# Kernel optimization log

Measured on AMD Instinct MI355X. Metric: run time of the kernel, lower is better.

## Reference

```python
import jax, jax.numpy as jnp
import numpy as np

B, N, K, H, HEADS = 4, 2000, 30, 128, 4
D = H // HEADS  # per-head dim = 32
NUM_IN = 2 * H
NEG_INF = jnp.float32(np.finfo(np.float32).min)


def setup_inputs() -> dict:
    key = jax.random.key(0)
    ks = jax.random.split(key, 10)
    h_V = jax.random.normal(ks[0], (B, N, H), jnp.float32)
    h_EV = jax.random.normal(ks[1], (B, N, K, NUM_IN), jnp.float32)
    h_KV = jax.random.normal(ks[2], (B, N, K, H), jnp.float32)
    h_KE = jax.random.normal(ks[3], (B, N, K, H), jnp.float32)
    mask_attend = (jax.random.uniform(ks[4], (B, N, K)) > 0.2).astype(jnp.float32)
    s = 1.0 / np.sqrt(H)
    W_Q = jax.random.normal(ks[5], (H, H), jnp.float32) * s
    W_K1 = jax.random.normal(ks[6], (H, H), jnp.float32) * s
    W_K2 = jax.random.normal(ks[7], (H, H), jnp.float32) * s
    W_V = jax.random.normal(ks[8], (H, NUM_IN), jnp.float32) * (1.0 / np.sqrt(NUM_IN))
    W_O = jax.random.normal(ks[9], (H, H), jnp.float32) * s
    return {"h_V": h_V, "h_EV": h_EV, "h_KV": h_KV, "h_KE": h_KE,
            "mask_attend": mask_attend, "W_Q": W_Q, "W_K1": W_K1,
            "W_K2": W_K2, "W_V": W_V, "W_O": W_O}


def reference(h_V, h_EV, h_KV, h_KE, mask_attend, W_Q, W_K1, W_K2, W_V, W_O):
    # Projections (torch Linear: y = x @ W.T)
    Q = (h_V @ W_Q.T).reshape(B, N, 1, HEADS, D)          # broadcast over K
    K1 = (h_KE @ W_K1.T).reshape(B, N, K, HEADS, D)
    K2 = (h_KV @ W_K2.T).reshape(B, N, K, HEADS, D)
    V = (h_EV @ W_V.T).reshape(B, N, K, HEADS, D)
    # Trilinear score: sum_d Q*K1*K2 -> [B,N,K,h] -> [B,N,h,K], scaled by 1/d
    logits = jnp.einsum('bnkhd,bnkhd->bnkh', Q * K1, K2)
    logits = jnp.transpose(logits, (0, 1, 3, 2)) / D      # [B,N,h,K]
    # Masked softmax over neighbor axis
    mask = jnp.broadcast_to(mask_attend[:, :, None, :], logits.shape)
    logits = jnp.where(mask > 0, logits, NEG_INF)
    attend = jax.nn.softmax(logits, axis=-1) * mask       # [B,N,h,K]
    # Weighted aggregation over neighbors
    h_upd = jnp.einsum('bnhk,bnkhd->bnhd', attend, V).reshape(B, N, H)
    return h_upd @ W_O.T
```

## Files before the change

### kernel.cpp

```cpp
#include <hip/hip_runtime.h>


#define KNB 30
#define HH 128
#define NUMIN 256
#define TOK 8000
#define TOTROW (TOK*KNB)
#define TILES 4
#define TOKB (2*TILES)
#define NBLK (TOK/TOKB)
#define SAW 136

typedef __bf16 bf16x8 __attribute__((ext_vector_type(8)));
typedef __bf16 bf16x4_t __attribute__((ext_vector_type(4)));
typedef float f32x4 __attribute__((ext_vector_type(4)));

__global__ __launch_bounds__(256) void conv_w_kernel(
    const float* __restrict__ wk1, const float* __restrict__ wk2,
    const float* __restrict__ wv, __bf16* __restrict__ ws) {
  int e = (blockIdx.x * 256 + threadIdx.x) * 4;
  const float* src; int off;
  if (e < 16384)      { src = wk1; off = e; }
  else if (e < 32768) { src = wk2; off = e - 16384; }
  else                { src = wv;  off = e - 32768; }
  float4 v = *(const float4*)(src + off);
  bf16x4_t o4;
  o4.x = (__bf16)v.x; o4.y = (__bf16)v.y; o4.z = (__bf16)v.z; o4.w = (__bf16)v.w;
  *(bf16x4_t*)(ws + e) = o4;
}

__global__ __launch_bounds__(256, 3) void na_main_kernel(
    const float* __restrict__ h_V, const float* __restrict__ h_EV,
    const float* __restrict__ h_KV, const float* __restrict__ h_KE,
    const float* __restrict__ maskp, const float* __restrict__ W_Q,
    const float* __restrict__ W_O, const __bf16* __restrict__ bW,
    float* __restrict__ out) {
  __shared__ __bf16 sA[2][64 * SAW];
  __shared__ float sQ[TOKB][HH];
  __shared__ float sU[TOKB][HH];
  __shared__ float sMask[TOKB][32];

  const int tid = threadIdx.x;
  const int lane = tid & 63;
  const int wave = tid >> 6;
  const int m = lane & 15;
  const int quad = lane >> 4;
  const int tok0 = blockIdx.x * TOKB;

  const __bf16* bWK1 = bW;
  const __bf16* bWK2 = bW + 16384;
  const __bf16* bWV  = bW + 32768;

  const int srow = tid >> 5;
  const int scol = (tid & 31) << 2;

  float4 svA[8], svB[8];

  auto stage_load = [&](float4 (&sv)[8], const float* base, int ld, int tile,
                        int coloff) {
    const long r0 = (long)(tok0 + 2 * tile) * KNB + srow;
#pragma unroll
    for (int j = 0; j < 8; j++) {
      long rr = r0 + j * 8;
      if (rr > TOTROW - 1) rr = TOTROW - 1;
      sv[j] = *(const float4*)(base + rr * (long)ld + coloff + scol);
    }
  };
  auto stage_store = [&](float4 (&sv)[8], int b) {
#pragma unroll
    for (int j = 0; j < 8; j++) {
      bf16x4_t o;
      o.x = (__bf16)sv[j].x; o.y = (__bf16)sv[j].y;
      o.z = (__bf16)sv[j].z; o.w = (__bf16)sv[j].w;
      *(bf16x4_t*)&sA[b][(srow + j * 8) * SAW + scol] = o;
    }
  };

  f32x4 accA[4][2], accB[4][2];
  const f32x4 fzero = {0.f, 0.f, 0.f, 0.f};
  auto gemm = [&](const __bf16* gW, int ldw, int kb, const __bf16* Ab,
                  f32x4 (*acc)[2]) {
#pragma unroll
    for (int ks = 0; ks < 4; ks++) {
      const int kc = kb + ks * 32 + quad * 8;
      bf16x8 b0 = *(const bf16x8*)(gW + (wave * 32 + m) * ldw + kc);
      bf16x8 b1 = *(const bf16x8*)(gW + (wave * 32 + 16 + m) * ldw + kc);
#pragma unroll
      for (int mt = 0; mt < 4; mt++) {
        bf16x8 a = *(const bf16x8*)&Ab[(mt * 16 + m) * SAW + ks * 32 + quad * 8];
        acc[mt][0] = __builtin_amdgcn_mfma_f32_16x16x32_bf16(a, b0, acc[mt][0], 0, 0, 0);
        acc[mt][1] = __builtin_amdgcn_mfma_f32_16x16x32_bf16(a, b1, acc[mt][1], 0, 0, 0);
      }
    }
  };

  stage_load(svB, h_KE, HH, 0, 0);
  stage_load(svA, h_KV, HH, 0, 0);
  if (tid < TOKB * KNB)
    sMask[tid / KNB][tid % KNB] = maskp[(long)tok0 * KNB + tid];
  {
    const int o = tid & 127, g = tid >> 7;
    const float4* wq = (const float4*)(W_Q + o * HH);
    float qa[4] = {0.f, 0.f, 0.f, 0.f};
#pragma unroll
    for (int j = 0; j < 32; j++) {
      float4 b = wq[j];
#pragma unroll
      for (int t = 0; t < 4; t++) {
        float4 a = *(const float4*)(h_V + (long)(tok0 + g * 4 + t) * HH + j * 4);
        qa[t] += a.x * b.x + a.y * b.y + a.z * b.z + a.w * b.w;
      }
    }
#pragma unroll
    for (int t = 0; t < 4; t++) sQ[g * 4 + t][o] = qa[t];
  }
  stage_store(svB, 0);
  __syncthreads();

  for (int it = 0; it < TILES; ++it) {
    const int tb = 2 * it;
    float lg[4][4];

    stage_load(svB, h_EV, NUMIN, it, 0);
#pragma unroll
    for (int mt = 0; mt < 4; mt++) { accA[mt][0] = fzero; accA[mt][1] = fzero; }
    gemm(bWK1, HH, 0, sA[0], accA);
    stage_store(svA, 1);
    __syncthreads();

    stage_load(svA, h_EV, NUMIN, it, 128);
#pragma unroll
    for (int mt = 0; mt < 4; mt++) { accB[mt][0] = fzero; accB[mt][1] = fzero; }
    gemm(bWK2, HH, 0, sA[1], accB);
#pragma unroll
    for (int mt = 0; mt < 4; mt++) {
      accA[mt][0] *= accB[mt][0];
      accA[mt][1] *= accB[mt][1];
    }
    {
      float q0[2], q1[2];
#pragma unroll
      for (int nt = 0; nt < 2; nt++) {
        q0[nt] = sQ[tb][wave * 32 + nt * 16 + m];
        q1[nt] = sQ[tb + 1][wave * 32 + nt * 16 + m];
      }
#pragma unroll
      for (int mt = 0; mt < 4; mt++)
#pragma unroll
        for (int r = 0; r < 4; r++) {
          int R = mt * 16 + quad * 4 + r;
          float qa0 = (R < 30) ? q0[0] : q1[0];
          float qa1 = (R < 30) ? q0[1] : q1[1];
          lg[mt][r] = accA[mt][0][r] * qa0 + accA[mt][1][r] * qa1;
        }
#pragma unroll
      for (int d = 1; d < 16; d <<= 1)
#pragma unroll
        for (int mt = 0; mt < 4; mt++)
#pragma unroll
          for (int r = 0; r < 4; r++)
            lg[mt][r] += __shfl_xor(lg[mt][r], d);

      float mx0 = -3.0e38f, mx1 = -3.0e38f;
#pragma unroll
      for (int mt = 0; mt < 4; mt++)
#pragma unroll
        for (int r = 0; r < 4; r++) {
          int R = mt * 16 + quad * 4 + r;
          if (R < 60) {
            int t = R >= 30, k = R - 30 * t;
            float l = (sMask[tb + t][k] > 0.f) ? lg[mt][r] * 0.03125f : -3.0e38f;
            lg[mt][r] = l;
            if (t == 0) mx0 = fmaxf(mx0, l); else mx1 = fmaxf(mx1, l);
          } else lg[mt][r] = -3.0e38f;
        }
      mx0 = fmaxf(mx0, __shfl_xor(mx0, 16)); mx0 = fmaxf(mx0, __shfl_xor(mx0, 32));
      mx1 = fmaxf(mx1, __shfl_xor(mx1, 16)); mx1 = fmaxf(mx1, __shfl_xor(mx1, 32));
      float s0 = 0.f, s1 = 0.f;
#pragma unroll
      for (int mt = 0; mt < 4; mt++)
#pragma unroll
        for (int r = 0; r < 4; r++) {
          int R = mt * 16 + quad * 4 + r;
          float e = 0.f;
          if (R < 60) {
            int t = R >= 30, k = R - 30 * t;
            if (sMask[tb + t][k] > 0.f) {
              float mxt = (t == 0) ? mx0 : mx1;
              e = __expf(lg[mt][r] - mxt);
            }
            if (t == 0) s0 += e; else s1 += e;
          }
          lg[mt][r] = e;
        }
      s0 += __shfl_xor(s0, 16); s0 += __shfl_xor(s0, 32);
      s1 += __shfl_xor(s1, 16); s1 += __shfl_xor(s1, 32);
      float inv0 = (s0 > 0.f) ? 1.f / s0 : 0.f;
      float inv1 = (s1 > 0.f) ? 1.f / s1 : 0.f;
#pragma unroll
      for (int mt = 0; mt < 4; mt++)
#pragma unroll
        for (int r = 0; r < 4; r++) {
          int R = mt * 16 + quad * 4 + r;
          lg[mt][r] *= (R < 30) ? inv0 : inv1;
        }
    }
    stage_store(svB, 0);
    __syncthreads();

    if (it + 1 < TILES) stage_load(svB, h_KE, HH, it + 1, 0);
#pragma unroll
    for (int mt = 0; mt < 4; mt++) { accB[mt][0] = fzero; accB[mt][1] = fzero; }
    gemm(bWV, NUMIN, 0, sA[0], accB);
    stage_store(svA, 1);
    __syncthreads();

    if (it + 1 < TILES) stage_load(svA, h_KV, HH, it + 1, 0);
    gemm(bWV, NUMIN, 128, sA[1], accB);
    {
      float u00 = 0.f, u01 = 0.f, u10 = 0.f, u11 = 0.f;
#pragma unroll
      for (int mt = 0; mt < 4; mt++)
#pragma unroll
        for (int r = 0; r < 4; r++) {
          int R = mt * 16 + quad * 4 + r;
          if (R < 30) {
            u00 += lg[mt][r] * accB[mt][0][r];
            u01 += lg[mt][r] * accB[mt][1][r];
          } else if (R < 60) {
            u10 += lg[mt][r] * accB[mt][0][r];
            u11 += lg[mt][r] * accB[mt][1][r];
          }
        }
      u00 += __shfl_xor(u00, 16); u00 += __shfl_xor(u00, 32);
      u01 += __shfl_xor(u01, 16); u01 += __shfl_xor(u01, 32);
      u10 += __shfl_xor(u10, 16); u10 += __shfl_xor(u10, 32);
      u11 += __shfl_xor(u11, 16); u11 += __shfl_xor(u11, 32);
      if (quad == 0) {
        sU[tb][wave * 32 + m]          = u00;
        sU[tb][wave * 32 + 16 + m]     = u01;
        sU[tb + 1][wave * 32 + m]      = u10;
        sU[tb + 1][wave * 32 + 16 + m] = u11;
      }
    }
    if (it + 1 < TILES) stage_store(svB, 0);
    __syncthreads();
  }

  {
    const int o = tid & 127, g = tid >> 7;
    const float4* wo = (const float4*)(W_O + o * HH);
    float r[4] = {0.f, 0.f, 0.f, 0.f};
#pragma unroll
    for (int j = 0; j < 32; j++) {
      float4 b = wo[j];
#pragma unroll
      for (int t = 0; t < 4; t++) {
        float4 a = *(const float4*)(&sU[g * 4 + t][j * 4]);
        r[t] += a.x * b.x + a.y * b.y + a.z * b.z + a.w * b.w;
      }
    }
#pragma unroll
    for (int t = 0; t < 4; t++)
      out[(long)(tok0 + g * 4 + t) * HH + o] = r[t];
  }
}

extern "C" void kernel_launch(void* const* d_in, const int* in_sizes, int n_in,
                              void* d_out, int out_size, void* d_ws, size_t ws_size,
                              hipStream_t stream) {
  const float* h_V  = (const float*)d_in[0];
  const float* h_EV = (const float*)d_in[1];
  const float* h_KV = (const float*)d_in[2];
  const float* h_KE = (const float*)d_in[3];
  const float* mask = (const float*)d_in[4];
  const float* W_Q  = (const float*)d_in[5];
  const float* W_K1 = (const float*)d_in[6];
  const float* W_K2 = (const float*)d_in[7];
  const float* W_V  = (const float*)d_in[8];
  const float* W_O  = (const float*)d_in[9];
  __bf16* bW = (__bf16*)d_ws;

  conv_w_kernel<<<64, 256, 0, stream>>>(W_K1, W_K2, W_V, bW);
  na_main_kernel<<<NBLK, 256, 0, stream>>>(h_V, h_EV, h_KV, h_KE, mask,
                                           W_Q, W_O, bW, (float*)d_out);
}
```

Before: 619.5 us.

## Load MFMA A operands directly from global memory instead of LDS staging

Removes the shared-memory staging buffers and the register prefetch pipeline for the h_KE, h_KV and h_EV tiles. Each wave now reads its A fragments straight from global fp32 and converts them to bf16 in registers right before each MFMA. This drops the intermediate syncthreads and the LDS footprint, which may allow more blocks to be resident. In exchange, every one of the four waves re-reads the same activation rows, so global and cache traffic rises about fourfold, and loads are no longer overlapped with the previous tile's compute.

```diff
diff --git a/kernel.cpp b/kernel.cpp
--- a/kernel.cpp
+++ b/kernel.cpp
@@ -9,7 +9,6 @@
 #define TILES 4
 #define TOKB (2*TILES)
 #define NBLK (TOK/TOKB)
-#define SAW 136
 
 typedef __bf16 bf16x8 __attribute__((ext_vector_type(8)));
 typedef __bf16 bf16x4_t __attribute__((ext_vector_type(4)));
@@ -29,13 +28,21 @@
   *(bf16x4_t*)(ws + e) = o4;
 }
 
+__device__ inline bf16x8 cvt8(const float* __restrict__ p) {
+  float4 a0 = *(const float4*)p;
+  float4 a1 = *(const float4*)(p + 4);
+  bf16x8 r;
+  r[0] = (__bf16)a0.x; r[1] = (__bf16)a0.y; r[2] = (__bf16)a0.z; r[3] = (__bf16)a0.w;
+  r[4] = (__bf16)a1.x; r[5] = (__bf16)a1.y; r[6] = (__bf16)a1.z; r[7] = (__bf16)a1.w;
+  return r;
+}
+
 __global__ __launch_bounds__(256, 3) void na_main_kernel(
     const float* __restrict__ h_V, const float* __restrict__ h_EV,
     const float* __restrict__ h_KV, const float* __restrict__ h_KE,
     const float* __restrict__ maskp, const float* __restrict__ W_Q,
     const float* __restrict__ W_O, const __bf16* __restrict__ bW,
     float* __restrict__ out) {
-  __shared__ __bf16 sA[2][64 * SAW];
   __shared__ float sQ[TOKB][HH];
   __shared__ float sU[TOKB][HH];
   __shared__ float sMask[TOKB][32];
@@ -51,51 +58,28 @@
   const __bf16* bWK2 = bW + 16384;
   const __bf16* bWV  = bW + 32768;
 
-  const int srow = tid >> 5;
-  const int scol = (tid & 31) << 2;
-
-  float4 svA[8], svB[8];
-
-  auto stage_load = [&](float4 (&sv)[8], const float* base, int ld, int tile,
-                        int coloff) {
-    const long r0 = (long)(tok0 + 2 * tile) * KNB + srow;
-#pragma unroll
-    for (int j = 0; j < 8; j++) {
-      long rr = r0 + j * 8;
-      if (rr > TOTROW - 1) rr = TOTROW - 1;
-      sv[j] = *(const float4*)(base + rr * (long)ld + coloff + scol);
-    }
-  };
-  auto stage_store = [&](float4 (&sv)[8], int b) {
-#pragma unroll
-    for (int j = 0; j < 8; j++) {
-      bf16x4_t o;
-      o.x = (__bf16)sv[j].x; o.y = (__bf16)sv[j].y;
-      o.z = (__bf16)sv[j].z; o.w = (__bf16)sv[j].w;
-      *(bf16x4_t*)&sA[b][(srow + j * 8) * SAW + scol] = o;
-    }
-  };
-
   f32x4 accA[4][2], accB[4][2];
   const f32x4 fzero = {0.f, 0.f, 0.f, 0.f};
-  auto gemm = [&](const __bf16* gW, int ldw, int kb, const __bf16* Ab,
-                  f32x4 (*acc)[2]) {
+
+  auto gemm_g = [&](const __bf16* gW, int ldw, int kw, const float* gA,
+                    int lda, int ka, int r0, f32x4 (*acc)[2]) {
 #pragma unroll
     for (int ks = 0; ks < 4; ks++) {
-      const int kc = kb + ks * 32 + quad * 8;
-      bf16x8 b0 = *(const bf16x8*)(gW + (wave * 32 + m) * ldw + kc);
-      bf16x8 b1 = *(const bf16x8*)(gW + (wave * 32 + 16 + m) * ldw + kc);
+      const int kcW = kw + ks * 32 + quad * 8;
+      bf16x8 b0 = *(const bf16x8*)(gW + (wave * 32 + m) * ldw + kcW);
+      bf16x8 b1 = *(const bf16x8*)(gW + (wave * 32 + 16 + m) * ldw + kcW);
 #pragma unroll
       for (int mt = 0; mt < 4; mt++) {
-        bf16x8 a = *(const bf16x8*)&Ab[(mt * 16 + m) * SAW + ks * 32 + quad * 8];
+        int rr = r0 + mt * 16 + m;
+        if (rr > TOTROW - 1) rr = TOTROW - 1;
+        const float* ap = gA + (long)rr * lda + ka + ks * 32 + quad * 8;
+        bf16x8 a = cvt8(ap);
         acc[mt][0] = __builtin_amdgcn_mfma_f32_16x16x32_bf16(a, b0, acc[mt][0], 0, 0, 0);
         acc[mt][1] = __builtin_amdgcn_mfma_f32_16x16x32_bf16(a, b1, acc[mt][1], 0, 0, 0);
       }
     }
   };
 
-  stage_load(svB, h_KE, HH, 0, 0);
-  stage_load(svA, h_KV, HH, 0, 0);
   if (tid < TOKB * KNB)
     sMask[tid / KNB][tid % KNB] = maskp[(long)tok0 * KNB + tid];
   {
@@ -114,29 +98,28 @@
 #pragma unroll
     for (int t = 0; t < 4; t++) sQ[g * 4 + t][o] = qa[t];
   }
-  stage_store(svB, 0);
   __syncthreads();
 
+#pragma unroll 1
   for (int it = 0; it < TILES; ++it) {
     const int tb = 2 * it;
+    const int r0 = (tok0 + 2 * it) * KNB;
     float lg[4][4];
 
-    stage_load(svB, h_EV, NUMIN, it, 0);
 #pragma unroll
     for (int mt = 0; mt < 4; mt++) { accA[mt][0] = fzero; accA[mt][1] = fzero; }
-    gemm(bWK1, HH, 0, sA[0], accA);
-    stage_store(svA, 1);
-    __syncthreads();
-
-    stage_load(svA, h_EV, NUMIN, it, 128);
+    gemm_g(bWK1, HH, 0, h_KE, HH, 0, r0, accA);
+
 #pragma unroll
     for (int mt = 0; mt < 4; mt++) { accB[mt][0] = fzero; accB[mt][1] = fzero; }
-    gemm(bWK2, HH, 0, sA[1], accB);
+    gemm_g(bWK2, HH, 0, h_KV, HH, 0, r0, accB);
+
 #pragma unroll
     for (int mt = 0; mt < 4; mt++) {
       accA[mt][0] *= accB[mt][0];
       accA[mt][1] *= accB[mt][1];
     }
+
     {
       float q0[2], q1[2];
 #pragma unroll
@@ -205,18 +188,12 @@
           lg[mt][r] *= (R < 30) ? inv0 : inv1;
         }
     }
-    stage_store(svB, 0);
-    __syncthreads();
-
-    if (it + 1 < TILES) stage_load(svB, h_KE, HH, it + 1, 0);
+
 #pragma unroll
     for (int mt = 0; mt < 4; mt++) { accB[mt][0] = fzero; accB[mt][1] = fzero; }
-    gemm(bWV, NUMIN, 0, sA[0], accB);
-    stage_store(svA, 1);
-    __syncthreads();
-
-    if (it + 1 < TILES) stage_load(svA, h_KV, HH, it + 1, 0);
-    gemm(bWV, NUMIN, 128, sA[1], accB);
+    gemm_g(bWV, NUMIN, 0,   h_EV, NUMIN, 0,   r0, accB);
+    gemm_g(bWV, NUMIN, 128, h_EV, NUMIN, 128, r0, accB);
+
     {
       float u00 = 0.f, u01 = 0.f, u10 = 0.f, u11 = 0.f;
 #pragma unroll
@@ -243,9 +220,8 @@
         sU[tb + 1][wave * 32 + 16 + m] = u11;
       }
     }
-    if (it + 1 < TILES) stage_store(svB, 0);
-    __syncthreads();
   }
+  __syncthreads();
 
   {
     const int o = tid & 127, g = tid >> 7;
```

New measurement: 801.3 us. 1.29x slower.
